# Optimization experiments

Hardware: AMD Instinct MI355X
Metric: run time of the kernel (lower is better)

The kernel has to match this reference:

```python
import jax, jax.numpy as jnp
import numpy as np

K = 16  # neighborhood size


def _eigen_ratio(pts, k):
    """pts: [B, N, 3] -> ratio lambda_max / lambda_mid per point, [B, N]."""
    pts = pts[..., :3]
    # pairwise squared distances [B, N, N]
    sq = jnp.sum(pts * pts, axis=-1)  # [B, N]
    d2 = sq[:, :, None] + sq[:, None, :] - 2.0 * jnp.einsum('bnd,bmd->bnm', pts, pts)
    # k nearest neighbors (self included, as in KNN(x, x))
    _, idx = jax.lax.top_k(-d2, k)  # idx: [B, N, k] int32
    # gather neighbor coordinates: [B, N, k, 3]
    neighbors = jax.vmap(lambda p, i: p[i])(pts, idx)
    mean = jnp.mean(neighbors, axis=2, keepdims=True)
    diff = neighbors - mean  # [B, N, k, 3]
    # covariance = mean over k of outer products -> [B, N, 3, 3]
    cov = jnp.einsum('bnki,bnkj->bnij', diff, diff) / k
    ev = jnp.linalg.eigvalsh(cov)  # ascending: [..., 3]
    return ev[..., 2] / ev[..., 1]


def setup_inputs() -> dict:
    key = jax.random.key(0)
    kx, ky = jax.random.split(key)
    x = jax.random.normal(kx, (2, 8192, 3), dtype=jnp.float32)
    y = jax.random.normal(ky, (2, 8192, 3), dtype=jnp.float32)
    return {"x": x, "y": y}


def reference(x, y):
    er1 = _eigen_ratio(x, K)  # [B, N]
    er2 = _eigen_ratio(y, K)
    res = jnp.mean((er1 - er2) ** 2, axis=-1)  # mean over points
    return jnp.mean(res)  # reduction='mean' over batch
```

## Files before the change

kernel.cpp:

```cpp
#include <hip/hip_runtime.h>
#include <hip/hip_bf16.h>
#include <math.h>

#define NPTS   8192
#define KNN    16
#define G      16
#define NCELL  (G * G * G)
#define NCHUNK 128
#define NPART  4

__constant__ float c_B[17] = {
    -1e30f,
    -1.5341205f, -1.1503494f, -0.8871466f, -0.6744898f, -0.4887764f,
    -0.3186394f, -0.1573107f,  0.0f,        0.1573107f,  0.3186394f,
     0.4887764f,  0.6744898f,  0.8871466f,  1.1503494f,  1.5341205f,
     1e30f
};

__device__ __forceinline__ int cellOf(float v) {
    int c = 0;
#pragma unroll
    for (int i = 1; i <= 15; ++i) c += (v >= c_B[i]) ? 1 : 0;
    return c;
}

__device__ __forceinline__ int spread3(int v) {
    v = (v | (v << 4)) & 0x0C3;
    v = (v | (v << 2)) & 0x249;
    return v;
}

__device__ __forceinline__ int mortonCell(float px, float py, float pz) {
    return (spread3(cellOf(px)) << 2) | (spread3(cellOf(py)) << 1) | spread3(cellOf(pz));
}

__device__ __forceinline__ float dpp_prev_f(float v) {
    int r = __builtin_amdgcn_update_dpp(0, __float_as_int(v), 0x111, 0xF, 0xF, false);
    return __int_as_float(r);
}
__device__ __forceinline__ int dpp_prev_i(int v) {
    return __builtin_amdgcn_update_dpp(0, v, 0x111, 0xF, 0xF, false);
}

__device__ __forceinline__ float sum16(float v) {
    int b;
    b = __builtin_amdgcn_update_dpp(0, __float_as_int(v), 0xB1, 0xF, 0xF, false);
    v += __int_as_float(b);
    b = __builtin_amdgcn_update_dpp(0, __float_as_int(v), 0x4E, 0xF, 0xF, false);
    v += __int_as_float(b);
    b = __builtin_amdgcn_update_dpp(0, __float_as_int(v), 0x141, 0xF, 0xF, false);
    v += __int_as_float(b);
    b = __builtin_amdgcn_update_dpp(0, __float_as_int(v), 0x140, 0xF, 0xF, false);
    v += __int_as_float(b);
    return v;
}

__global__ __launch_bounds__(256) void count_kernel(
    const float* __restrict__ x, const float* __restrict__ y,
    unsigned int* __restrict__ cellcnt) {

    __shared__ unsigned int h[NCELL];
    const int tid   = threadIdx.x;
    const int cloud = blockIdx.x >> 2;
    const int part  = blockIdx.x & 3;
    const float* __restrict__ src = (cloud < 2 ? x : y) + (size_t)(cloud & 1) * NPTS * 3;

    for (int i = tid; i < NCELL; i += 256) h[i] = 0;
    __syncthreads();
#pragma unroll
    for (int k = 0; k < 8; ++k) {
        int p = (part << 11) | (k << 8) | tid;
        atomicAdd(&h[mortonCell(src[3 * p], src[3 * p + 1], src[3 * p + 2])], 1u);
    }
    __syncthreads();
    unsigned int* cc = cellcnt + (cloud * NPART + part) * NCELL;
    for (int i = tid; i < NCELL; i += 256) cc[i] = h[i];
}

__global__ __launch_bounds__(1024) void scan_kernel(unsigned int* __restrict__ cellcnt) {
    __shared__ unsigned int scanbuf[1024];
    const int tid = threadIdx.x;
    unsigned int* cc = cellcnt + blockIdx.x * (NPART * NCELL);

    unsigned int v[NPART][4], csum[4];
    unsigned int ssum = 0;
#pragma unroll
    for (int j = 0; j < 4; ++j) {
        int cell = 4 * tid + j;
        unsigned int s = 0;
#pragma unroll
        for (int p = 0; p < NPART; ++p) { v[p][j] = cc[p * NCELL + cell]; s += v[p][j]; }
        csum[j] = s; ssum += s;
    }
    scanbuf[tid] = ssum;
    __syncthreads();
    for (int d = 1; d < 1024; d <<= 1) {
        unsigned int a = scanbuf[tid];
        unsigned int w = (tid >= d) ? scanbuf[tid - d] : 0;
        __syncthreads();
        scanbuf[tid] = a + w;
        __syncthreads();
    }
    unsigned int run = scanbuf[tid] - ssum;
#pragma unroll
    for (int j = 0; j < 4; ++j) {
        int cell = 4 * tid + j;
        unsigned int pr = run;
#pragma unroll
        for (int p = 0; p < NPART; ++p) { cc[p * NCELL + cell] = pr; pr += v[p][j]; }
        run += csum[j];
    }
}

__global__ __launch_bounds__(256) void scatter_kernel(
    const float* __restrict__ x, const float* __restrict__ y,
    unsigned int* __restrict__ cellcnt,
    float4* __restrict__ Ps, unsigned short* __restrict__ origids) {

    const int tid   = threadIdx.x;
    const int cloud = blockIdx.x >> 2;
    const int part  = blockIdx.x & 3;
    const float* __restrict__ src = (cloud < 2 ? x : y) + (size_t)(cloud & 1) * NPTS * 3;
    unsigned int* cc = cellcnt + (cloud * NPART + part) * NCELL;

#pragma unroll
    for (int k = 0; k < 8; ++k) {
        int p = (part << 11) | (k << 8) | tid;
        float px = src[3 * p], py = src[3 * p + 1], pz = src[3 * p + 2];
        int c = mortonCell(px, py, pz);
        unsigned int pos = atomicAdd(&cc[c], 1u);
        Ps[(cloud << 13) + pos] = make_float4(-2.f * px, -2.f * py, -2.f * pz,
                                              px * px + py * py + pz * pz);
        origids[(cloud << 13) + pos] = (unsigned short)p;
    }
}

__global__ __launch_bounds__(256) void aabb_kernel(
    const float4* __restrict__ Ps, float* __restrict__ aabbG ) {

    const int tid  = threadIdx.x;
    const int lane = tid & 63;
    const int w    = (blockIdx.x << 2) | (tid >> 6);
    const int cloud = w >> 7;
    const int c     = w & 127;

    float4 f = Ps[(cloud << 13) | (c << 6) | lane];
    float px = -0.5f * f.x, py = -0.5f * f.y, pz = -0.5f * f.z;
    float lx = px, hx = px, ly = py, hy = py, lz = pz, hz = pz;
#pragma unroll
    for (int s = 1; s < 64; s <<= 1) {
        lx = fminf(lx, __shfl_xor(lx, s)); hx = fmaxf(hx, __shfl_xor(hx, s));
        ly = fminf(ly, __shfl_xor(ly, s)); hy = fmaxf(hy, __shfl_xor(hy, s));
        lz = fminf(lz, __shfl_xor(lz, s)); hz = fmaxf(hz, __shfl_xor(hz, s));
    }
    if (lane == 0) {
        float* ab = aabbG + cloud * (6 * NCHUNK);
        ab[0 * NCHUNK + c] = lx; ab[1 * NCHUNK + c] = hx;
        ab[2 * NCHUNK + c] = ly; ab[3 * NCHUNK + c] = hy;
        ab[4 * NCHUNK + c] = lz; ab[5 * NCHUNK + c] = hz;
    }
}

__global__ __launch_bounds__(64) void knn_cov_kernel(
    const float4* __restrict__ Ps, const unsigned short* __restrict__ origids,
    const float* __restrict__ aabbG, float* __restrict__ er) {

    const int lane = threadIdx.x;
    const int wid  = blockIdx.x;
    const int cloud = wid >> 13;
    const int s     = wid & (NPTS - 1);

    const float4* __restrict__ Pc = Ps + (cloud << 13);
    const float* __restrict__ ab = aabbG + cloud * (6 * NCHUNK);
    const float4 qp = Pc[s];
    const float sqq = qp.w;
    const float qx = -0.5f * qp.x, qy = -0.5f * qp.y, qz = -0.5f * qp.z;
    const int co = s >> 6;

    float bval[2];
#pragma unroll
    for (int g = 0; g < 2; ++g) {
        int c = (g << 6) | lane;
        float dxl = fmaxf(0.f, fmaxf(ab[c] - qx, qx - ab[NCHUNK + c]));
        float dyl = fmaxf(0.f, fmaxf(ab[2 * NCHUNK + c] - qy, qy - ab[3 * NCHUNK + c]));
        float dzl = fmaxf(0.f, fmaxf(ab[4 * NCHUNK + c] - qz, qz - ab[5 * NCHUNK + c]));
        bval[g] = dxl * dxl + dyl * dyl + dzl * dzl;
    }
    unsigned long long rem0 = ~0ull, rem1 = ~0ull;
    if (co < 64) rem0 &= ~(1ull << co); else rem1 &= ~(1ull << (co - 64));

    auto dual_argmin = [&](unsigned long long live0, unsigned long long live1,
                           int& cidA, int& cidB, bool& hasB) {
        unsigned int k0 = ((live0 >> lane) & 1)
            ? ((__float_as_uint(bval[0]) & 0xFFFFFF80u) | (unsigned)lane) : 0xFFFFFFFFu;
        unsigned int k1 = ((live1 >> lane) & 1)
            ? ((__float_as_uint(bval[1]) & 0xFFFFFF80u) | (unsigned)(64 + lane)) : 0xFFFFFFFFu;
        unsigned int a = min(k0, k1), b = max(k0, k1);
#pragma unroll
        for (int w = 1; w < 64; w <<= 1) {
            unsigned int oa = __shfl_xor(a, w);
            unsigned int ob = __shfl_xor(b, w);
            unsigned int mn = min(a, oa), mx = max(a, oa);
            unsigned int c2 = (a < oa) ? b : ob;
            a = mn; b = min(mx, c2);
        }
        cidA = (int)(a & 127u);
        hasB = (b != 0xFFFFFFFFu); cidB = (int)(b & 127u);
    };
    auto clear_rem = [&](int cid) {
        if (cid < 64) rem0 &= ~(1ull << cid); else rem1 &= ~(1ull << (cid - 64));
    };
    auto bound_of = [&](int cid) {
        return __int_as_float(__builtin_amdgcn_readlane(
            __float_as_int(bval[cid >> 6]), cid & 63));
    };

    int pA, pB; bool hB;
    dual_argmin(rem0, rem1, pA, pB, hB);
    clear_rem(pA); clear_rem(pB);
    float4 pfA = Pc[(pA << 6) | lane];
    float4 pfB = Pc[(pB << 6) | lane];

    float valV, thr;
    int   idxV;
    {
        int pos = (co << 6) | lane;
        float4 f = Pc[pos];
        float k = fmaf(qx, f.x, fmaf(qy, f.y, fmaf(qz, f.z, sqq + f.w)));
        int p = pos;
#pragma unroll
        for (int size = 2; size <= 64; size <<= 1) {
#pragma unroll
            for (int stride = size >> 1; stride >= 1; stride >>= 1) {
                float ok = __shfl_xor(k, stride);
                int   op = __shfl_xor(p, stride);
                bool up = ((lane & size) == 0);
                bool lower = ((lane & stride) == 0);
                bool want_min = (up == lower);
                bool take = want_min ? (ok < k) : (ok > k);
                k = take ? ok : k;
                p = take ? op : p;
            }
        }
        valV = __shfl(k, lane & 15);
        idxV = __shfl(p, lane & 15);
        thr  = __shfl(k, 15);
    }

    auto process = [&](float4 f, int cid) {
        float d2 = fmaf(qx, f.x, fmaf(qy, f.y, fmaf(qz, f.z, sqq + f.w)));
        unsigned long long m = __ballot(d2 < thr);
        if (m) {
            do {
                int li = __builtin_ctzll(m); m &= m - 1;
                float sv = __int_as_float(
                    __builtin_amdgcn_readlane(__float_as_int(d2), li));
                int sj = (cid << 6) | li;
                float pv = dpp_prev_f(valV);
                int   pi = dpp_prev_i(idxV);
                bool keep  = (valV <= sv);
                bool fromv = ((lane & 15) == 0) || (pv <= sv);
                float nv = keep ? valV : (fromv ? sv : pv);
                int   ni = keep ? idxV : (fromv ? sj : pi);
                valV = nv; idxV = ni;
            } while (m);
            thr = __int_as_float(__builtin_amdgcn_readlane(__float_as_int(valV), 15));
        }
    };

    if (bound_of(pA) < thr) process(pfA, pA);
    if (bound_of(pB) < thr) process(pfB, pB);

    for (;;) {
        unsigned long long live0 = rem0 & __ballot(bval[0] < thr);
        unsigned long long live1 = rem1 & __ballot(bval[1] < thr);
        if (!(live0 | live1)) break;

        int cidA, cidB; bool hasB;
        if (__popcll(live0) + __popcll(live1) <= 2) {
            if (live0) { cidA = __builtin_ctzll(live0); live0 &= live0 - 1; }
            else       { cidA = 64 + __builtin_ctzll(live1); live1 &= live1 - 1; }
            if (live0)      { cidB = __builtin_ctzll(live0); hasB = true; }
            else if (live1) { cidB = 64 + __builtin_ctzll(live1); hasB = true; }
            else hasB = false;
        } else {
            dual_argmin(live0, live1, cidA, cidB, hasB);
        }
        clear_rem(cidA);
        if (hasB) clear_rem(cidB);

        float4 fA = Pc[(cidA << 6) | lane];
        float4 fB;
        if (hasB) fB = Pc[(cidB << 6) | lane];

        process(fA, cidA);
        if (hasB && bound_of(cidB) < thr) process(fB, cidB);
    }

    float4 nf = Pc[idxV];
    float nx = -0.5f * nf.x, ny = -0.5f * nf.y, nz = -0.5f * nf.z;

    const float invk = 1.0f / KNN;
    float mx = sum16(nx) * invk;
    float my = sum16(ny) * invk;
    float mz = sum16(nz) * invk;

    float dx = nx - mx, dy = ny - my, dz = nz - mz;
    float c00 = sum16(dx * dx) * invk, c01 = sum16(dx * dy) * invk, c02 = sum16(dx * dz) * invk;
    float c11 = sum16(dy * dy) * invk, c12 = sum16(dy * dz) * invk, c22 = sum16(dz * dz) * invk;

    double a00 = c00, a01 = c01, a02 = c02, a11 = c11, a12 = c12, a22 = c22;
    double qm = (a00 + a11 + a22) * (1.0 / 3.0);
    double p1 = a01 * a01 + a02 * a02 + a12 * a12;
    double b00 = a00 - qm, b11 = a11 - qm, b22 = a22 - qm;
    double p2 = b00 * b00 + b11 * b11 + b22 * b22 + 2.0 * p1;

    double ratio;
    if (p2 <= 0.0) {
        ratio = 1.0;
    } else {
        double p = sqrt(p2 * (1.0 / 6.0));
        double inv = 1.0 / p;
        double m00 = b00 * inv, m11 = b11 * inv, m22 = b22 * inv;
        double m01 = a01 * inv, m02 = a02 * inv, m12 = a12 * inv;
        double detB = m00 * (m11 * m22 - m12 * m12)
                    - m01 * (m01 * m22 - m12 * m02)
                    + m02 * (m01 * m12 - m11 * m02);
        double r = 0.5 * detB;
        r = fmin(1.0, fmax(-1.0, r));
        double phi = acos(r) * (1.0 / 3.0);
        double e1 = qm + 2.0 * p * cos(phi);
        double e3 = qm + 2.0 * p * cos(phi + 2.0943951023931953);
        double e2 = 3.0 * qm - e1 - e3;
        ratio = e1 / e2;
    }

    if (lane == 0) {
        int orig = origids[(cloud << 13) + s];
        er[(cloud << 13) + orig] = (float)ratio;
    }
}

__global__ __launch_bounds__(1024) void final_kernel(const float* __restrict__ er,
                                                     float* __restrict__ out) {
    __shared__ double sb[1024];
    double acc = 0.0;
    const int total = 2 * NPTS;
    for (int i = threadIdx.x; i < total; i += 1024) {
        double d = (double)er[i] - (double)er[total + i];
        acc += d * d;
    }
    sb[threadIdx.x] = acc;
    __syncthreads();
    for (int s2 = 512; s2 > 0; s2 >>= 1) {
        if (threadIdx.x < s2) sb[threadIdx.x] += sb[threadIdx.x + s2];
        __syncthreads();
    }
    if (threadIdx.x == 0) out[0] = (float)(sb[0] / (double)total);
}

extern "C" void kernel_launch(void* const* d_in, const int* in_sizes, int n_in,
                              void* d_out, int out_size, void* d_ws, size_t ws_size,
                              hipStream_t stream) {
    const float* x = (const float*)d_in[0];
    const float* y = (const float*)d_in[1];
    char* ws = (char*)d_ws;

    float4*         Ps      = (float4*)(ws);
    unsigned short* origids = (unsigned short*)(ws + 524288);
    float*          aabbG   = (float*)(ws + 589824);
    float*          er      = (float*)(ws + 602112);
    unsigned int*   cellcnt = (unsigned int*)(ws + 733184);
    float*          out     = (float*)d_out;

    count_kernel<<<4 * NPART, 256, 0, stream>>>(x, y, cellcnt);
    scan_kernel<<<4, 1024, 0, stream>>>(cellcnt);
    scatter_kernel<<<4 * NPART, 256, 0, stream>>>(x, y, cellcnt, Ps, origids);
    aabb_kernel<<<128, 256, 0, stream>>>(Ps, aabbG);
    knn_cov_kernel<<<4 * NPTS, 64, 0, stream>>>(Ps, origids, aabbG, er);
    final_kernel<<<1, 1024, 0, stream>>>(er, out);
}
```

Baseline: 102.3 us.

## Merge count and scan kernels; move eigen-solve out of KNN into reduction kernel

The per-cell count and the prefix scan now run in one kernel with one block per cloud, which drops the per-part histogram split and one launch. The scatter kernel's blocks for a cloud now share a single per-cloud offset table through atomics. The KNN kernel no longer computes the fp64 closed-form eigenvalue ratio, which every lane of every wave was evaluating redundantly. It writes the 6 covariance terms instead, and a new kernel computes the ratios one thread per point and reduces them in blocks, followed by a 64-lane final sum. This trades extra covariance traffic through global memory and an extra launch for far less fp64 trig work and lower register pressure in the main kernel.

```diff
diff --git a/kernel.cpp b/kernel.cpp
--- a/kernel.cpp
+++ b/kernel.cpp
@@ -55,43 +55,28 @@
     return v;
 }
 
-__global__ __launch_bounds__(256) void count_kernel(
+__global__ __launch_bounds__(1024) void countscan_kernel(
     const float* __restrict__ x, const float* __restrict__ y,
-    unsigned int* __restrict__ cellcnt) {
+    unsigned int* __restrict__ cellcnt ) {
 
     __shared__ unsigned int h[NCELL];
+    __shared__ unsigned int scanbuf[1024];
     const int tid   = threadIdx.x;
-    const int cloud = blockIdx.x >> 2;
-    const int part  = blockIdx.x & 3;
+    const int cloud = blockIdx.x;
     const float* __restrict__ src = (cloud < 2 ? x : y) + (size_t)(cloud & 1) * NPTS * 3;
 
-    for (int i = tid; i < NCELL; i += 256) h[i] = 0;
+    for (int i = tid; i < NCELL; i += 1024) h[i] = 0;
     __syncthreads();
 #pragma unroll
     for (int k = 0; k < 8; ++k) {
-        int p = (part << 11) | (k << 8) | tid;
+        int p = (k << 10) | tid;
         atomicAdd(&h[mortonCell(src[3 * p], src[3 * p + 1], src[3 * p + 2])], 1u);
     }
     __syncthreads();
-    unsigned int* cc = cellcnt + (cloud * NPART + part) * NCELL;
-    for (int i = tid; i < NCELL; i += 256) cc[i] = h[i];
-}
-
-__global__ __launch_bounds__(1024) void scan_kernel(unsigned int* __restrict__ cellcnt) {
-    __shared__ unsigned int scanbuf[1024];
-    const int tid = threadIdx.x;
-    unsigned int* cc = cellcnt + blockIdx.x * (NPART * NCELL);
-
-    unsigned int v[NPART][4], csum[4];
-    unsigned int ssum = 0;
-#pragma unroll
-    for (int j = 0; j < 4; ++j) {
-        int cell = 4 * tid + j;
-        unsigned int s = 0;
-#pragma unroll
-        for (int p = 0; p < NPART; ++p) { v[p][j] = cc[p * NCELL + cell]; s += v[p][j]; }
-        csum[j] = s; ssum += s;
-    }
+
+    unsigned int c0 = h[4 * tid], c1 = h[4 * tid + 1];
+    unsigned int c2 = h[4 * tid + 2], c3 = h[4 * tid + 3];
+    unsigned int ssum = c0 + c1 + c2 + c3;
     scanbuf[tid] = ssum;
     __syncthreads();
     for (int d = 1; d < 1024; d <<= 1) {
@@ -101,15 +86,12 @@
         scanbuf[tid] = a + w;
         __syncthreads();
     }
-    unsigned int run = scanbuf[tid] - ssum;
-#pragma unroll
-    for (int j = 0; j < 4; ++j) {
-        int cell = 4 * tid + j;
-        unsigned int pr = run;
-#pragma unroll
-        for (int p = 0; p < NPART; ++p) { cc[p * NCELL + cell] = pr; pr += v[p][j]; }
-        run += csum[j];
-    }
+    unsigned int excl = scanbuf[tid] - ssum;
+    unsigned int* cc = cellcnt + cloud * NCELL;
+    cc[4 * tid]     = excl;
+    cc[4 * tid + 1] = excl + c0;
+    cc[4 * tid + 2] = excl + c0 + c1;
+    cc[4 * tid + 3] = excl + c0 + c1 + c2;
 }
 
 __global__ __launch_bounds__(256) void scatter_kernel(
@@ -121,7 +103,7 @@
     const int cloud = blockIdx.x >> 2;
     const int part  = blockIdx.x & 3;
     const float* __restrict__ src = (cloud < 2 ? x : y) + (size_t)(cloud & 1) * NPTS * 3;
-    unsigned int* cc = cellcnt + (cloud * NPART + part) * NCELL;
+    unsigned int* cc = cellcnt + cloud * NCELL;
 
 #pragma unroll
     for (int k = 0; k < 8; ++k) {
@@ -163,7 +145,7 @@
 
 __global__ __launch_bounds__(64) void knn_cov_kernel(
     const float4* __restrict__ Ps, const unsigned short* __restrict__ origids,
-    const float* __restrict__ aabbG, float* __restrict__ er) {
+    const float* __restrict__ aabbG, float* __restrict__ cov) {
 
     const int lane = threadIdx.x;
     const int wid  = blockIdx.x;
@@ -309,54 +291,63 @@
     float c00 = sum16(dx * dx) * invk, c01 = sum16(dx * dy) * invk, c02 = sum16(dx * dz) * invk;
     float c11 = sum16(dy * dy) * invk, c12 = sum16(dy * dz) * invk, c22 = sum16(dz * dz) * invk;
 
-    double a00 = c00, a01 = c01, a02 = c02, a11 = c11, a12 = c12, a22 = c22;
+    if (lane == 0) {
+        int orig = origids[(cloud << 13) + s];
+        float* cp = cov + ((size_t)(cloud << 13) + orig) * 6;
+        *(float2*)(cp)     = make_float2(c00, c01);
+        *(float2*)(cp + 2) = make_float2(c02, c11);
+        *(float2*)(cp + 4) = make_float2(c12, c22);
+    }
+}
+
+__device__ double eig_ratio(const float* __restrict__ cp) {
+    double a00 = cp[0], a01 = cp[1], a02 = cp[2];
+    double a11 = cp[3], a12 = cp[4], a22 = cp[5];
+
     double qm = (a00 + a11 + a22) * (1.0 / 3.0);
     double p1 = a01 * a01 + a02 * a02 + a12 * a12;
     double b00 = a00 - qm, b11 = a11 - qm, b22 = a22 - qm;
     double p2 = b00 * b00 + b11 * b11 + b22 * b22 + 2.0 * p1;
 
-    double ratio;
-    if (p2 <= 0.0) {
-        ratio = 1.0;
-    } else {
-        double p = sqrt(p2 * (1.0 / 6.0));
-        double inv = 1.0 / p;
-        double m00 = b00 * inv, m11 = b11 * inv, m22 = b22 * inv;
-        double m01 = a01 * inv, m02 = a02 * inv, m12 = a12 * inv;
-        double detB = m00 * (m11 * m22 - m12 * m12)
-                    - m01 * (m01 * m22 - m12 * m02)
-                    + m02 * (m01 * m12 - m11 * m02);
-        double r = 0.5 * detB;
-        r = fmin(1.0, fmax(-1.0, r));
-        double phi = acos(r) * (1.0 / 3.0);
-        double e1 = qm + 2.0 * p * cos(phi);
-        double e3 = qm + 2.0 * p * cos(phi + 2.0943951023931953);
-        double e2 = 3.0 * qm - e1 - e3;
-        ratio = e1 / e2;
-    }
-
-    if (lane == 0) {
-        int orig = origids[(cloud << 13) + s];
-        er[(cloud << 13) + orig] = (float)ratio;
-    }
-}
-
-__global__ __launch_bounds__(1024) void final_kernel(const float* __restrict__ er,
-                                                     float* __restrict__ out) {
-    __shared__ double sb[1024];
-    double acc = 0.0;
-    const int total = 2 * NPTS;
-    for (int i = threadIdx.x; i < total; i += 1024) {
-        double d = (double)er[i] - (double)er[total + i];
-        acc += d * d;
-    }
-    sb[threadIdx.x] = acc;
+    if (p2 <= 0.0) return 1.0;
+    double p = sqrt(p2 * (1.0 / 6.0));
+    double inv = 1.0 / p;
+    double m00 = b00 * inv, m11 = b11 * inv, m22 = b22 * inv;
+    double m01 = a01 * inv, m02 = a02 * inv, m12 = a12 * inv;
+    double detB = m00 * (m11 * m22 - m12 * m12)
+                - m01 * (m01 * m22 - m12 * m02)
+                + m02 * (m01 * m12 - m11 * m02);
+    double r = 0.5 * detB;
+    r = fmin(1.0, fmax(-1.0, r));
+    double phi = acos(r) * (1.0 / 3.0);
+    double e1 = qm + 2.0 * p * cos(phi);
+    double e3 = qm + 2.0 * p * cos(phi + 2.0943951023931953);
+    double e2 = 3.0 * qm - e1 - e3;
+    return e1 / e2;
+}
+
+__global__ __launch_bounds__(256) void eigred_kernel(const float* __restrict__ cov,
+                                                     double* __restrict__ partial) {
+    __shared__ double sb[256];
+    const int i = blockIdx.x * 256 + threadIdx.x;
+    double r1 = eig_ratio(cov + (size_t)i * 6);
+    double r2 = eig_ratio(cov + (size_t)(2 * NPTS + i) * 6);
+    double d = r1 - r2;
+    sb[threadIdx.x] = d * d;
     __syncthreads();
-    for (int s2 = 512; s2 > 0; s2 >>= 1) {
+    for (int s2 = 128; s2 > 0; s2 >>= 1) {
         if (threadIdx.x < s2) sb[threadIdx.x] += sb[threadIdx.x + s2];
         __syncthreads();
     }
-    if (threadIdx.x == 0) out[0] = (float)(sb[0] / (double)total);
+    if (threadIdx.x == 0) partial[blockIdx.x] = sb[0];
+}
+
+__global__ __launch_bounds__(64) void final_kernel(const double* __restrict__ partial,
+                                                   float* __restrict__ out) {
+    double v = partial[threadIdx.x];
+#pragma unroll
+    for (int w = 1; w < 64; w <<= 1) v += __shfl_xor(v, w);
+    if (threadIdx.x == 0) out[0] = (float)(v / (double)(2 * NPTS));
 }
 
 extern "C" void kernel_launch(void* const* d_in, const int* in_sizes, int n_in,
@@ -369,14 +360,15 @@
     float4*         Ps      = (float4*)(ws);
     unsigned short* origids = (unsigned short*)(ws + 524288);
     float*          aabbG   = (float*)(ws + 589824);
-    float*          er      = (float*)(ws + 602112);
-    unsigned int*   cellcnt = (unsigned int*)(ws + 733184);
+    float*          cov     = (float*)(ws + 602112);
+    unsigned int*   cellcnt = (unsigned int*)(ws + 1388544);
+    double*         partial = (double*)(ws + 1454080);
     float*          out     = (float*)d_out;
 
-    count_kernel<<<4 * NPART, 256, 0, stream>>>(x, y, cellcnt);
-    scan_kernel<<<4, 1024, 0, stream>>>(cellcnt);
+    countscan_kernel<<<4, 1024, 0, stream>>>(x, y, cellcnt);
     scatter_kernel<<<4 * NPART, 256, 0, stream>>>(x, y, cellcnt, Ps, origids);
     aabb_kernel<<<128, 256, 0, stream>>>(Ps, aabbG);
-    knn_cov_kernel<<<4 * NPTS, 64, 0, stream>>>(Ps, origids, aabbG, er);
-    final_kernel<<<1, 1024, 0, stream>>>(er, out);
-}
+    knn_cov_kernel<<<4 * NPTS, 64, 0, stream>>>(Ps, origids, aabbG, cov);
+    eigred_kernel<<<64, 256, 0, stream>>>(cov, partial);
+    final_kernel<<<1, 64, 0, stream>>>(partial, out);
+}
```

Result: faster. 90.08 us (-11.9%).
